# Kernel optimization log

Hardware: AMD Instinct MI355X
Metric: run time of the kernel (lower is better)

Reference implementation:

```python
import jax, jax.numpy as jnp
import numpy as np

B, N, C, H, E = 4, 10000, 128, 128, 160000


def setup_inputs() -> dict:
    key = jax.random.key(0)
    ks = jax.random.split(key, 16)
    d_in = C + H
    s = 1.0 / np.sqrt(d_in)
    inp = {
        "x": jax.random.normal(ks[0], (B, N, C), jnp.float32),
        "h": jax.random.normal(ks[1], (B, N, H), jnp.float32),
        "c": jax.random.normal(ks[2], (B, N, H), jnp.float32),
        "edge_index": jax.random.randint(ks[3], (2, E), 0, N, jnp.int64),
        "edge_weight": jax.random.uniform(ks[4], (E,), jnp.float32),
        "W_i": jax.random.uniform(ks[5], (d_in, H), jnp.float32, -s, s),
        "b_i": jnp.zeros((H,), jnp.float32),
        "W_f": jax.random.uniform(ks[6], (d_in, H), jnp.float32, -s, s),
        "b_f": jnp.zeros((H,), jnp.float32),
        "W_o": jax.random.uniform(ks[7], (d_in, H), jnp.float32, -s, s),
        "b_o": jnp.zeros((H,), jnp.float32),
        "W_g": jax.random.uniform(ks[8], (d_in, H), jnp.float32, -s, s),
        "b_g": jnp.zeros((H,), jnp.float32),
    }
    return inp


def reference(x, h, c, edge_index, edge_weight, W_i, b_i, W_f, b_f, W_o, b_o, W_g, b_g):
    n = x.shape[1]
    hid = W_i.shape[1]
    src, dst = edge_index[0], edge_index[1]
    # GCNConv: add self-loops (weight 1.0) and symmetric normalization
    loop = jnp.arange(n)
    src_a = jnp.concatenate([src, loop])
    dst_a = jnp.concatenate([dst, loop])
    w_a = jnp.concatenate([edge_weight, jnp.ones((n,), edge_weight.dtype)])
    deg = jax.ops.segment_sum(w_a, dst_a, num_segments=n)  # [N]
    dinv = jnp.where(deg > 0, jax.lax.rsqrt(deg), 0.0)
    norm = dinv[src_a] * w_a * dinv[dst_a]  # [E+N]

    xh = jnp.concatenate([x, h], axis=-1)  # [B, N, C+H]
    # Fuse the four gate convs: same edge_index/normalization, shared gather-scatter
    W = jnp.concatenate([W_i, W_f, W_o, W_g], axis=1)  # [C+H, 4H]
    b = jnp.concatenate([b_i, b_f, b_o, b_g])  # [4H]
    xt = jnp.einsum("bnd,dh->bnh", xh, W)  # [B, N, 4H]
    msgs = xt[:, src_a, :] * norm[None, :, None]  # [B, E+N, 4H]
    agg = jnp.zeros_like(xt).at[:, dst_a, :].add(msgs) + b  # [B, N, 4H]

    i = jax.nn.sigmoid(agg[..., 0 * hid:1 * hid])
    f = jax.nn.sigmoid(agg[..., 1 * hid:2 * hid])
    o = jax.nn.sigmoid(agg[..., 2 * hid:3 * hid])
    g = jnp.tanh(agg[..., 3 * hid:4 * hid])
    c_new = f * c + i * g
    h_new = o * jnp.tanh(c_new)
    return h_new, c_new
```

## Files before the change

kernel.cpp:

```cpp
#include <hip/hip_runtime.h>
#include <math.h>

#define NB 4
#define NN 10000
#define NE 160000
#define DIN 256
#define DOUT 512
#define SLOTS 48

typedef _Float16 f16x8 __attribute__((ext_vector_type(8)));
typedef _Float16 f16x2 __attribute__((ext_vector_type(2)));
typedef float f32x4 __attribute__((ext_vector_type(4)));

struct hv4 { f16x2 p[4]; };

#define GLOAD_LDS16(g, l) \
    __builtin_amdgcn_global_load_lds((const __attribute__((address_space(1))) void*)(g), \
                                     (__attribute__((address_space(3))) void*)(l), 16, 0, 0)

__global__ __launch_bounds__(256) void k_zero(int4* __restrict__ p) {
    p[blockIdx.x * 256 + threadIdx.x] = make_int4(0, 0, 0, 0);
}

__global__ __launch_bounds__(256) void k_packcvt(
        const float* __restrict__ Wi, const float* __restrict__ Wf,
        const float* __restrict__ Wo, const float* __restrict__ Wg,
        const float* __restrict__ bi, const float* __restrict__ bf,
        const float* __restrict__ bo, const float* __restrict__ bg,
        const int* __restrict__ ei, const float* __restrict__ ew,
        const float* __restrict__ x, const float* __restrict__ h,
        float* __restrict__ deg,
        _Float16* __restrict__ Wt2, float* __restrict__ bcat,
        _Float16* __restrict__ xhb, int4* __restrict__ ebuf4) {
    int bid = blockIdx.x;
    int t = threadIdx.x;
    if (bid < 512) {
        int i = bid * 256 + t;
        int e = i & 7;
        int j = (i >> 3) & 127;
        int lk = (i >> 10) & 3;
        int kb = (i >> 12) & 7;
        int g = i >> 15;
        const float* W = (g == 0) ? Wi : (g == 1) ? Wf : (g == 2) ? Wo : Wg;
        Wt2[i] = (_Float16)W[(kb * 32 + lk * 8 + e) * 128 + j];
        if (i < DOUT) {
            int gg = i >> 7, jj = i & 127;
            const float* bb = (gg == 0) ? bi : (gg == 1) ? bf : (gg == 2) ? bo : bg;
            bcat[i] = bb[jj];
        }
    } else if (bid < 1137) {
        int e = (bid - 512) * 256 + t;
        int dst = ei[NE + e];
        atomicAdd(&deg[dst], ew[e]);
    } else if (bid < 6137) {
        int id = (bid - 1137) * 256 + t;
        int f8 = id * 8;
        int row = f8 >> 8;
        int col = f8 & 255;
        int n = row >> 2, b = row & 3;
        const float* src = ((col >> 7) ? h : x) + ((size_t)b * NN + n) * 128 + (col & 127);
        float4 v0 = *(const float4*)src;
        float4 v1 = *(const float4*)(src + 4);
        f16x8 o;
        o[0] = (_Float16)v0.x; o[1] = (_Float16)v0.y;
        o[2] = (_Float16)v0.z; o[3] = (_Float16)v0.w;
        o[4] = (_Float16)v1.x; o[5] = (_Float16)v1.y;
        o[6] = (_Float16)v1.z; o[7] = (_Float16)v1.w;
        *(f16x8*)(xhb + (size_t)f8) = o;
    } else {
        int id = (bid - 6137) * 256 + t;
        if (id < NN * SLOTS / 2) ebuf4[id] = make_int4(0, 0, 0, 0);
    }
}

__global__ __launch_bounds__(256) void k_fill(const int* __restrict__ ei,
                                              const float* __restrict__ ew,
                                              const float* __restrict__ deg,
                                              int* cursor, int2* __restrict__ ebuf) {
    int e = blockIdx.x * 256 + threadIdx.x;
    int src = ei[e], dst = ei[NE + e];
    float norm = rsqrtf(deg[src] + 1.0f) * ew[e] * rsqrtf(deg[dst] + 1.0f);
    unsigned short hw;
    {
        _Float16 hnorm = (_Float16)norm;
        hw = __builtin_bit_cast(unsigned short, hnorm);
    }
    int wpair = (int)hw | ((int)hw << 16);
    int pos = atomicAdd(&cursor[dst], 1);
    if (pos < SLOTS) ebuf[dst * SLOTS + pos] = make_int2(src * 2048, wpair);
}

__global__ __launch_bounds__(512) void k_agg(const _Float16* __restrict__ xhb,
                                             const float* __restrict__ deg,
                                             const int* __restrict__ cursor,
                                             const int2* __restrict__ ebuf,
                                             _Float16* __restrict__ aggb) {
    int t = threadIdx.x;
    int lane = t & 63, wid = t >> 6;
    int bid = blockIdx.x;
    int xcd = bid & 7;
    int b = xcd >> 1, kh = xcd & 1;
    int n = (bid >> 3) * 8 + wid;
    int eg = lane >> 4;
    int fl16 = (lane & 15) << 4;

    const char* bbf = (const char*)xhb + (b << 9) + (kh << 8) + fl16;

    int2 epl = ebuf[(size_t)n * SLOTS + lane];
    hv4 vS = *(const hv4*)(bbf + n * 2048);
    float di = rsqrtf(deg[n] + 1.0f);
    int cnt = cursor[n];

    f16x2 pac0 = (f16x2)0, pac1 = (f16x2)0, pac2 = (f16x2)0, pac3 = (f16x2)0;

#define BPX(IDX) __builtin_amdgcn_ds_bpermute((IDX) << 2, epl.x)
#define BPY(IDX) __builtin_amdgcn_ds_bpermute((IDX) << 2, epl.y)
#define ACCH(EX, EY, V)                                     \
    {                                                       \
        f16x2 w2 = __builtin_bit_cast(f16x2, (EY));         \
        pac0 = (V).p[0] * w2 + pac0;                        \
        pac1 = (V).p[1] * w2 + pac1;                        \
        pac2 = (V).p[2] * w2 + pac2;                        \
        pac3 = (V).p[3] * w2 + pac3;                        \
    }

    int nw = (cnt + 15) >> 4;
    int idx = eg;
    for (int w = 0; w < nw; ++w, idx += 16) {
        int x0 = BPX(idx), y0 = BPY(idx);
        int x1 = BPX(idx + 4), y1 = BPY(idx + 4);
        int x2 = BPX(idx + 8), y2 = BPY(idx + 8);
        int x3 = BPX(idx + 12), y3 = BPY(idx + 12);
        hv4 v0 = *(const hv4*)(bbf + x0);
        hv4 v1 = *(const hv4*)(bbf + x1);
        hv4 v2 = *(const hv4*)(bbf + x2);
        hv4 v3 = *(const hv4*)(bbf + x3);
        ACCH(x0, y0, v0);
        ACCH(x1, y1, v1);
        ACCH(x2, y2, v2);
        ACCH(x3, y3, v3);
    }

#define PRED(P)                                                               \
    P = P + __builtin_bit_cast(f16x2, __shfl_xor(__builtin_bit_cast(int, P), 16)); \
    P = P + __builtin_bit_cast(f16x2, __shfl_xor(__builtin_bit_cast(int, P), 32));
    PRED(pac0) PRED(pac1) PRED(pac2) PRED(pac3)

    float a[8];
    a[0] = (float)pac0[0]; a[1] = (float)pac0[1];
    a[2] = (float)pac1[0]; a[3] = (float)pac1[1];
    a[4] = (float)pac2[0]; a[5] = (float)pac2[1];
    a[6] = (float)pac3[0]; a[7] = (float)pac3[1];
    {
        float wl = di * di;
        a[0] = fmaf(wl, (float)vS.p[0][0], a[0]);
        a[1] = fmaf(wl, (float)vS.p[0][1], a[1]);
        a[2] = fmaf(wl, (float)vS.p[1][0], a[2]);
        a[3] = fmaf(wl, (float)vS.p[1][1], a[3]);
        a[4] = fmaf(wl, (float)vS.p[2][0], a[4]);
        a[5] = fmaf(wl, (float)vS.p[2][1], a[5]);
        a[6] = fmaf(wl, (float)vS.p[3][0], a[6]);
        a[7] = fmaf(wl, (float)vS.p[3][1], a[7]);
    }
    if (eg == 0) {
        f16x8 o;
#pragma unroll
        for (int i = 0; i < 8; ++i) o[i] = (_Float16)a[i];
        *(f16x8*)(aggb + ((size_t)b * NN + n) * 256 + (kh << 7) + (fl16 >> 1)) = o;
    }
}

__global__ __launch_bounds__(256, 2) void k_gemm(const _Float16* __restrict__ aggb,
                                                 const _Float16* __restrict__ Wt2,
                                                 const float* __restrict__ bcat,
                                                 const float* __restrict__ c_in,
                                                 float* __restrict__ out) {
    __shared__ __align__(16) _Float16 sA[64 * 256];
    int t = threadIdx.x;
    int lane = t & 63, wid = t >> 6;
    int lr = lane & 15, lk = lane >> 4;
    int bid = blockIdx.x;
    int rb = bid >> 1, jb = bid & 1;
    int rowbase = rb * 64;
    int jj = jb * 64 + wid * 16 + lr;

    float cv[4][4];
#pragma unroll
    for (int mi = 0; mi < 4; ++mi)
#pragma unroll
        for (int r = 0; r < 4; ++r)
            cv[mi][r] = c_in[(size_t)(rowbase + mi * 16 + lk * 4 + r) * 128 + jj];

#pragma unroll
    for (int i = 0; i < 8; ++i) {
        int idx = i * 256 + t;
        int row = idx >> 5;
        int cb = (idx & 31) << 4;
        const char* g = (const char*)aggb + (size_t)(rowbase + row) * 512 + (cb ^ ((row & 7) << 4));
        char* l = (char*)sA + (size_t)(i * 256 + wid * 64) * 16;
        GLOAD_LDS16(g, l);
    }

    f16x8 breg[4][8];
#pragma unroll
    for (int g = 0; g < 4; ++g)
#pragma unroll
        for (int kb = 0; kb < 8; ++kb)
            breg[g][kb] = *(const f16x8*)(Wt2 + ((size_t)((g * 8 + kb) * 4 + lk) * 128 + jj) * 8);

    float b_i = bcat[jj], b_f = bcat[128 + jj], b_o = bcat[256 + jj], b_g = bcat[384 + jj];

    __syncthreads();

    f32x4 acc[4][4];
#pragma unroll
    for (int mi = 0; mi < 4; ++mi)
#pragma unroll
        for (int g = 0; g < 4; ++g) acc[mi][g] = (f32x4)0.f;

    int aswz = (lr & 7) << 4;
#pragma unroll
    for (int kb = 0; kb < 8; ++kb) {
        int koff = (kb << 6) + (lk << 4);
#pragma unroll
        for (int mi = 0; mi < 4; ++mi) {
            f16x8 a = *(const f16x8*)((const char*)sA + (mi * 16 + lr) * 512 + (koff ^ aswz));
            acc[mi][0] = __builtin_amdgcn_mfma_f32_16x16x32_f16(a, breg[0][kb], acc[mi][0], 0, 0, 0);
            acc[mi][1] = __builtin_amdgcn_mfma_f32_16x16x32_f16(a, breg[1][kb], acc[mi][1], 0, 0, 0);
            acc[mi][2] = __builtin_amdgcn_mfma_f32_16x16x32_f16(a, breg[2][kb], acc[mi][2], 0, 0, 0);
            acc[mi][3] = __builtin_amdgcn_mfma_f32_16x16x32_f16(a, breg[3][kb], acc[mi][3], 0, 0, 0);
        }
    }

#pragma unroll
    for (int mi = 0; mi < 4; ++mi) {
#pragma unroll
        for (int r = 0; r < 4; ++r) {
            int row = rowbase + mi * 16 + lk * 4 + r;
            size_t o = (size_t)row * 128 + jj;
            float vi = acc[mi][0][r] + b_i;
            float vf = acc[mi][1][r] + b_f;
            float vo = acc[mi][2][r] + b_o;
            float vg = acc[mi][3][r] + b_g;
            float ig = 1.f / (1.f + __expf(-vi));
            float fg = 1.f / (1.f + __expf(-vf));
            float og = 1.f / (1.f + __expf(-vo));
            float gg = 1.f - 2.f / (__expf(2.f * vg) + 1.f);
            float cn = fg * cv[mi][r] + ig * gg;
            float tc = 1.f - 2.f / (__expf(2.f * cn) + 1.f);
            out[o] = og * tc;
            out[(size_t)NB * NN * 128 + o] = cn;
        }
    }
}


extern "C" void kernel_launch(void* const* d_in, const int* in_sizes, int n_in,
                              void* d_out, int out_size, void* d_ws, size_t ws_size,
                              hipStream_t stream) {
    const float* x = (const float*)d_in[0];
    const float* h = (const float*)d_in[1];
    const float* c = (const float*)d_in[2];
    const int* ei = (const int*)d_in[3];
    const float* ew = (const float*)d_in[4];
    const float* Wi = (const float*)d_in[5];
    const float* bi = (const float*)d_in[6];
    const float* Wf = (const float*)d_in[7];
    const float* bf = (const float*)d_in[8];
    const float* Wo = (const float*)d_in[9];
    const float* bo = (const float*)d_in[10];
    const float* Wg = (const float*)d_in[11];
    const float* bg = (const float*)d_in[12];
    float* out = (float*)d_out;

    char* ws = (char*)d_ws;
    size_t off = 0;
    auto alloc = [&](size_t bytes) {
        void* p = ws + off;
        off = (off + bytes + 255) & ~(size_t)255;
        return p;
    };
    float* deg = (float*)alloc((size_t)NN * 4);
    int* cursor = (int*)alloc((size_t)NN * 4);
    float* bcat = (float*)alloc((size_t)DOUT * 4);
    _Float16* Wt2 = (_Float16*)alloc((size_t)DOUT * DIN * 2);
    int2* ebuf = (int2*)alloc((size_t)NN * SLOTS * 8 + 512);
    _Float16* xhb = (_Float16*)alloc((size_t)NN * 4 * DIN * 2);
    _Float16* aggb = (_Float16*)alloc((size_t)NB * NN * DIN * 2);

    hipLaunchKernelGGL(k_zero, dim3(20), dim3(256), 0, stream, (int4*)deg);

    hipLaunchKernelGGL(k_packcvt, dim3(7075), dim3(256), 0, stream,
                       Wi, Wf, Wo, Wg, bi, bf, bo, bg, ei, ew, x, h, deg, Wt2, bcat, xhb,
                       (int4*)ebuf);
    hipLaunchKernelGGL(k_fill, dim3(625), dim3(256), 0, stream,
                       ei, ew, deg, cursor, ebuf);
    hipLaunchKernelGGL(k_agg, dim3(10000), dim3(512), 0, stream,
                       xhb, deg, cursor, ebuf, aggb);
    hipLaunchKernelGGL(k_gemm, dim3(1250), dim3(256), 0, stream,
                       aggb, Wt2, bcat, c, out);
}
```

Baseline: 102.5 us.

## Make GEMM kernel persistent with double-buffered LDS staging of row chunks

The gate GEMM kernel now launches 512 persistent blocks instead of 1250. Each block handles 2-3 chunks of 64 rows, reuses its register-resident weight fragments across chunks, and prefetches the next chunk's A tile into a second LDS buffer while computing the current one. This is meant to amortise the per-block weight loads and hide global-to-LDS latency. In exchange it doubles LDS use per block (64 KB), which may reduce occupancy, and the chunk counts are unbalanced across blocks.

Result: no change. 103.4 us (+0.9%).

```diff
diff --git a/kernel.cpp b/kernel.cpp
--- a/kernel.cpp
+++ b/kernel.cpp
@@ -175,31 +175,30 @@
                                                  const float* __restrict__ bcat,
                                                  const float* __restrict__ c_in,
                                                  float* __restrict__ out) {
-    __shared__ __align__(16) _Float16 sA[64 * 256];
+    __shared__ __align__(16) _Float16 sA[2][64 * 256];
     int t = threadIdx.x;
     int lane = t & 63, wid = t >> 6;
     int lr = lane & 15, lk = lane >> 4;
     int bid = blockIdx.x;
-    int rb = bid >> 1, jb = bid & 1;
-    int rowbase = rb * 64;
+    int jb = bid & 1, slot = bid >> 1;
     int jj = jb * 64 + wid * 16 + lr;
-
-    float cv[4][4];
-#pragma unroll
-    for (int mi = 0; mi < 4; ++mi)
-#pragma unroll
-        for (int r = 0; r < 4; ++r)
-            cv[mi][r] = c_in[(size_t)(rowbase + mi * 16 + lk * 4 + r) * 128 + jj];
-
-#pragma unroll
-    for (int i = 0; i < 8; ++i) {
-        int idx = i * 256 + t;
-        int row = idx >> 5;
-        int cb = (idx & 31) << 4;
-        const char* g = (const char*)aggb + (size_t)(rowbase + row) * 512 + (cb ^ ((row & 7) << 4));
-        char* l = (char*)sA + (size_t)(i * 256 + wid * 64) * 16;
-        GLOAD_LDS16(g, l);
-    }
+    int nc = (slot < 113) ? 3 : 2;
+
+#define STAGE(BUF, CHUNK)                                                                  \
+    {                                                                                      \
+        _Pragma("unroll")                                                                  \
+        for (int i = 0; i < 8; ++i) {                                                      \
+            int idx = i * 256 + t;                                                         \
+            int row = idx >> 5;                                                            \
+            int cb = (idx & 31) << 4;                                                      \
+            const char* g = (const char*)aggb + (size_t)((CHUNK) * 64 + row) * 512 +       \
+                            (cb ^ ((row & 7) << 4));                                       \
+            char* l = (char*)&sA[(BUF)][0] + (size_t)(i * 256 + wid * 64) * 16;            \
+            GLOAD_LDS16(g, l);                                                             \
+        }                                                                                  \
+    }
+
+    STAGE(0, slot);
 
     f16x8 breg[4][8];
 #pragma unroll
@@ -210,46 +209,60 @@
 
     float b_i = bcat[jj], b_f = bcat[128 + jj], b_o = bcat[256 + jj], b_g = bcat[384 + jj];
 
-    __syncthreads();
-
-    f32x4 acc[4][4];
-#pragma unroll
-    for (int mi = 0; mi < 4; ++mi)
-#pragma unroll
-        for (int g = 0; g < 4; ++g) acc[mi][g] = (f32x4)0.f;
-
     int aswz = (lr & 7) << 4;
-#pragma unroll
-    for (int kb = 0; kb < 8; ++kb) {
-        int koff = (kb << 6) + (lk << 4);
+    for (int ci = 0; ci < nc; ++ci) {
+        int chunk = slot + ci * 256;
+        int buf = ci & 1;
+        __syncthreads();
+
+        float cv[4][4];
+#pragma unroll
+        for (int mi = 0; mi < 4; ++mi)
+#pragma unroll
+            for (int r = 0; r < 4; ++r)
+                cv[mi][r] = c_in[(size_t)(chunk * 64 + mi * 16 + lk * 4 + r) * 128 + jj];
+
+        if (ci + 1 < nc) STAGE(buf ^ 1, slot + (ci + 1) * 256);
+
+        f32x4 acc[4][4];
+#pragma unroll
+        for (int mi = 0; mi < 4; ++mi)
+#pragma unroll
+            for (int g = 0; g < 4; ++g) acc[mi][g] = (f32x4)0.f;
+
+        const char* sAb = (const char*)&sA[buf][0];
+#pragma unroll
+        for (int kb = 0; kb < 8; ++kb) {
+            int koff = (kb << 6) + (lk << 4);
+#pragma unroll
+            for (int mi = 0; mi < 4; ++mi) {
+                f16x8 a = *(const f16x8*)(sAb + (mi * 16 + lr) * 512 + (koff ^ aswz));
+                acc[mi][0] = __builtin_amdgcn_mfma_f32_16x16x32_f16(a, breg[0][kb], acc[mi][0], 0, 0, 0);
+                acc[mi][1] = __builtin_amdgcn_mfma_f32_16x16x32_f16(a, breg[1][kb], acc[mi][1], 0, 0, 0);
+                acc[mi][2] = __builtin_amdgcn_mfma_f32_16x16x32_f16(a, breg[2][kb], acc[mi][2], 0, 0, 0);
+                acc[mi][3] = __builtin_amdgcn_mfma_f32_16x16x32_f16(a, breg[3][kb], acc[mi][3], 0, 0, 0);
+            }
+        }
+
 #pragma unroll
         for (int mi = 0; mi < 4; ++mi) {
-            f16x8 a = *(const f16x8*)((const char*)sA + (mi * 16 + lr) * 512 + (koff ^ aswz));
-            acc[mi][0] = __builtin_amdgcn_mfma_f32_16x16x32_f16(a, breg[0][kb], acc[mi][0], 0, 0, 0);
-            acc[mi][1] = __builtin_amdgcn_mfma_f32_16x16x32_f16(a, breg[1][kb], acc[mi][1], 0, 0, 0);
-            acc[mi][2] = __builtin_amdgcn_mfma_f32_16x16x32_f16(a, breg[2][kb], acc[mi][2], 0, 0, 0);
-            acc[mi][3] = __builtin_amdgcn_mfma_f32_16x16x32_f16(a, breg[3][kb], acc[mi][3], 0, 0, 0);
-        }
-    }
-
-#pragma unroll
-    for (int mi = 0; mi < 4; ++mi) {
-#pragma unroll
-        for (int r = 0; r < 4; ++r) {
-            int row = rowbase + mi * 16 + lk * 4 + r;
-            size_t o = (size_t)row * 128 + jj;
-            float vi = acc[mi][0][r] + b_i;
-            float vf = acc[mi][1][r] + b_f;
-            float vo = acc[mi][2][r] + b_o;
-            float vg = acc[mi][3][r] + b_g;
-            float ig = 1.f / (1.f + __expf(-vi));
-            float fg = 1.f / (1.f + __expf(-vf));
-            float og = 1.f / (1.f + __expf(-vo));
-            float gg = 1.f - 2.f / (__expf(2.f * vg) + 1.f);
-            float cn = fg * cv[mi][r] + ig * gg;
-            float tc = 1.f - 2.f / (__expf(2.f * cn) + 1.f);
-            out[o] = og * tc;
-            out[(size_t)NB * NN * 128 + o] = cn;
+#pragma unroll
+            for (int r = 0; r < 4; ++r) {
+                int row = chunk * 64 + mi * 16 + lk * 4 + r;
+                size_t o = (size_t)row * 128 + jj;
+                float vi = acc[mi][0][r] + b_i;
+                float vf = acc[mi][1][r] + b_f;
+                float vo = acc[mi][2][r] + b_o;
+                float vg = acc[mi][3][r] + b_g;
+                float ig = 1.f / (1.f + __expf(-vi));
+                float fg = 1.f / (1.f + __expf(-vf));
+                float og = 1.f / (1.f + __expf(-vo));
+                float gg = 1.f - 2.f / (__expf(2.f * vg) + 1.f);
+                float cn = fg * cv[mi][r] + ig * gg;
+                float tc = 1.f - 2.f / (__expf(2.f * cn) + 1.f);
+                out[o] = og * tc;
+                out[(size_t)NB * NN * 128 + o] = cn;
+            }
         }
     }
 }
@@ -297,6 +310,6 @@
                        ei, ew, deg, cursor, ebuf);
     hipLaunchKernelGGL(k_agg, dim3(10000), dim3(512), 0, stream,
                        xhb, deg, cursor, ebuf, aggb);
-    hipLaunchKernelGGL(k_gemm, dim3(1250), dim3(256), 0, stream,
+    hipLaunchKernelGGL(k_gemm, dim3(512), dim3(256), 0, stream,
                        aggb, Wt2, bcat, c, out);
 }
```
